# Performance work log

Measured on AMD Instinct MI355X. Metric: run time of the kernel, lower is better.

## Reference

```python
import jax, jax.numpy as jnp
import numpy as np
from math import sqrt

B, S, D, H, E, K, FF = 2, 1024, 1024, 16, 8, 2, 4096
HD = D // H  # 64
EPS = 1e-5


def setup_inputs() -> dict:
    key = jax.random.key(0)
    ks = jax.random.split(key, 20)
    std = 0.02
    p = lambda k, sh: (jax.random.normal(k, sh, dtype=jnp.float32) * std)
    return {
        'x':  jax.random.normal(ks[0], (B, S, D), dtype=jnp.float32),
        'Wq': p(ks[1], (D, D)), 'bq': jnp.zeros((D,), jnp.float32),
        'Wk': p(ks[2], (D, D)), 'bk': jnp.zeros((D,), jnp.float32),
        'Wv': p(ks[3], (D, D)), 'bv': jnp.zeros((D,), jnp.float32),
        'Wo': p(ks[4], (D, D)), 'bo': jnp.zeros((D,), jnp.float32),
        'Wg': p(ks[5], (D, E)), 'bg': jnp.zeros((E,), jnp.float32),
        'W1': p(ks[6], (E, D, FF)), 'b1': jnp.zeros((E, FF), jnp.float32),
        'W2': p(ks[7], (E, FF, D)), 'b2': jnp.zeros((E, D), jnp.float32),
        'g1': jnp.ones((D,), jnp.float32), 'be1': jnp.zeros((D,), jnp.float32),
        'g2': jnp.ones((D,), jnp.float32), 'be2': jnp.zeros((D,), jnp.float32),
    }


def _rope_cache(seq_len, hd):
    inv_freq = 1.0 / (10000.0 ** (jnp.arange(0, hd, 2, dtype=jnp.float32) / hd))
    t = jnp.arange(seq_len, dtype=jnp.float32)
    freqs = t[:, None] * inv_freq[None, :]          # [S, hd/2]
    emb = jnp.concatenate([freqs, freqs], axis=-1)  # [S, hd]
    return jnp.cos(emb), jnp.sin(emb)


def _rotate_half(x):
    x1, x2 = jnp.split(x, 2, axis=-1)
    return jnp.concatenate([-x2, x1], axis=-1)


def _layernorm(x, g, b):
    m = jnp.mean(x, axis=-1, keepdims=True)
    v = jnp.var(x, axis=-1, keepdims=True)
    return (x - m) * jax.lax.rsqrt(v + EPS) * g + b


def _forward(x, Wq, bq, Wk, bk, Wv, bv, Wo, bo, Wg, bg, W1, b1, W2, b2, g1, be1, g2, be2):
    bsz, seq, d = x.shape
    # --- self-attention with RoPE (mask=None -> k=v=q=x) ---
    q = (x @ Wq + bq).reshape(bsz, seq, H, HD).transpose(0, 2, 1, 3)  # [B,H,S,hd]
    k = (x @ Wk + bk).reshape(bsz, seq, H, HD).transpose(0, 2, 1, 3)
    v = (x @ Wv + bv).reshape(bsz, seq, H, HD).transpose(0, 2, 1, 3)
    cos, sin = _rope_cache(seq, HD)                 # [S,hd]
    cos = cos[None, None]; sin = sin[None, None]
    q = q * cos + _rotate_half(q) * sin
    k = k * cos + _rotate_half(k) * sin
    scores = jnp.einsum('bhqd,bhkd->bhqk', q, k) / sqrt(HD)
    attn = jax.nn.softmax(scores, axis=-1)
    ao = jnp.einsum('bhqk,bhkd->bhqd', attn, v)
    ao = ao.transpose(0, 2, 1, 3).reshape(bsz, seq, d)
    attn_out = ao @ Wo + bo
    x1 = _layernorm(x + attn_out, g1, be1)
    # --- MoE: top-k routing, dense-equivalent weighted expert mixture ---
    gate_logits = x1 @ Wg + bg                      # [B,S,E]
    gate_probs = jax.nn.softmax(gate_logits, axis=-1)
    topk_p, topk_i = jax.lax.top_k(gate_probs, K)   # [B,S,K]
    topk_p = topk_p / jnp.sum(topk_p, axis=-1, keepdims=True)
    comb = jnp.sum(jax.nn.one_hot(topk_i, E, dtype=x.dtype) * topk_p[..., None], axis=-2)  # [B,S,E]
    h = jax.nn.gelu(jnp.einsum('bsd,edf->bsef', x1, W1) + b1, approximate=False)  # [B,S,E,FF]
    y = jnp.einsum('bsef,efd->bsed', h, W2) + b2    # [B,S,E,D]
    moe_out = jnp.einsum('bse,bsed->bsd', comb, y)
    return _layernorm(x1 + moe_out, g2, be2)


def reference(x, Wq, bq, Wk, bk, Wv, bv, Wo, bo, Wg, bg, W1, b1, W2, b2, g1, be1, g2, be2):
    return _forward(x, Wq, bq, Wk, bk, Wv, bv, Wo, bo, Wg, bg, W1, b1, W2, b2, g1, be1, g2, be2)
```

## Files before the change

### kernel.cpp

```cpp
#include <hip/hip_runtime.h>
#include <cmath>

#define Bz 2
#define Sz 1024
#define Dz 1024
#define Hz 16
#define HDz 64
#define Ez 8
#define FFz 4096
#define Nz (Bz*Sz)
#define SLOTSz (2*Nz)
#define QKVSz (3*Dz)
#define EPSz 1e-5f
#define NRB 40

typedef __attribute__((ext_vector_type(8))) short bf16x8;
typedef __attribute__((ext_vector_type(4))) short bf16x4;
typedef __attribute__((ext_vector_type(4))) float f32x4;
typedef __attribute__((ext_vector_type(8))) unsigned short ushortx8;

__device__ __forceinline__ float b2f(unsigned short u){
  union { unsigned int i; float f; } x; x.i = ((unsigned int)u) << 16; return x.f;
}
__device__ __forceinline__ unsigned short f2b(float f){
  union { float f; unsigned int i; } x; x.f = f;
  unsigned int r = x.i + 0x7FFFu + ((x.i >> 16) & 1u);
  return (unsigned short)(r >> 16);
}
__device__ __forceinline__ float erf_fast(float x){
  float ax = fabsf(x);
  float t = 1.0f/(1.0f + 0.3275911f*ax);
  float p = t*(0.254829592f + t*(-0.284496736f + t*(1.421413741f +
            t*(-1.453152027f + t*1.061405429f))));
  float r = 1.0f - p*__expf(-ax*ax);
  return copysignf(r, x);
}
__device__ __forceinline__ float gelu_f(float x){
  return 0.5f*x*(1.0f + erf_fast(x*0.70710678118654752f));
}
__device__ __forceinline__ void gload16(const void* g, void* l){
  __builtin_amdgcn_global_load_lds(
    (const __attribute__((address_space(1))) unsigned int*)g,
    (__attribute__((address_space(3))) unsigned int*)l, 16, 0, 0);
}

__device__ __forceinline__ void transpose_body(
    const float* __restrict__ in, unsigned short* __restrict__ out,
    int R, int C, int bx, int by, int tid, float (*tile)[65])
{
  int c0 = bx*64, r0 = by*64;
  int tx = tid & 15, ty = tid >> 4;
  #pragma unroll
  for (int i = 0; i < 4; ++i) {
    float4 v = *(const float4*)(in + (size_t)(r0+ty+16*i)*C + c0 + tx*4);
    tile[ty+16*i][tx*4+0] = v.x; tile[ty+16*i][tx*4+1] = v.y;
    tile[ty+16*i][tx*4+2] = v.z; tile[ty+16*i][tx*4+3] = v.w;
  }
  __syncthreads();
  int oc = tid >> 3, og = tid & 7;
  #pragma unroll
  for (int p = 0; p < 2; ++p) {
    int c = oc + p*32;
    ushortx8 u;
    #pragma unroll
    for (int j = 0; j < 8; ++j) u[j] = f2b(tile[og*8+j][c]);
    *(ushortx8*)(out + (size_t)(c0+c)*R + r0 + og*8) = u;
  }
}

__global__ __launch_bounds__(256) void prologue_k(
    const float* __restrict__ Wq, const float* __restrict__ Wk,
    const float* __restrict__ Wv, const float* __restrict__ Wo,
    const float* __restrict__ bq, const float* __restrict__ bk,
    const float* __restrict__ bv, const float* __restrict__ x,
    unsigned short* __restrict__ Wqt, unsigned short* __restrict__ Wkt,
    unsigned short* __restrict__ Wvt, unsigned short* __restrict__ Wot,
    float* __restrict__ bqkv, unsigned short* __restrict__ xb,
    int* __restrict__ counts)
{
  __shared__ float tile[64][65];
  int id = blockIdx.x, t = threadIdx.x;
  if (id < 1024) {
    int which = id >> 8, rem = id & 255;
    const float* in = (which==0)?Wq:(which==1)?Wk:(which==2)?Wv:Wo;
    unsigned short* out = (which==0)?Wqt:(which==1)?Wkt:(which==2)?Wvt:Wot;
    transpose_body(in, out, Dz, Dz, rem & 15, rem >> 4, t, tile);
  } else if (id < 1024 + 2048) {
    int i = ((id-1024)*256 + t)*4;
    float4 v = *(const float4*)(x + i);
    ushort4 o; o.x=f2b(v.x); o.y=f2b(v.y); o.z=f2b(v.z); o.w=f2b(v.w);
    *(ushort4*)(xb + i) = o;
  } else {
    int i = (id - 3072)*256 + t;
    if (i < 3072) bqkv[i] = (i < 1024) ? bq[i] : (i < 2048 ? bk[i-1024] : bv[i-2048]);
    if (id == 3072 && t < Ez) counts[t] = 0;
  }
}

__device__ __forceinline__ void mfma_kloop(
    const unsigned short* __restrict__ pA0, const unsigned short* __restrict__ pA1,
    const unsigned short* __restrict__ pB0, const unsigned short* __restrict__ pB1,
    char* lds, int t, int K, f32x4 acc[4][4])
{
  const int lane = t & 63, w = t >> 6;
  const int wrOff = (w >> 1) * 4096;
  const int wcOff = (w & 1) * 4096;
  const int lr = lane & 15, q = lane >> 4;
  const int xq = (q ^ (lr & 3)) << 4;
  const int baseA = wrOff + lr*64 + xq;
  const int baseB = 8192 + wcOff + lr*64 + xq;
  for (int k0 = 0; k0 < K; k0 += 32) {
    __syncthreads();
    gload16(pA0 + k0, lds + t*16);
    gload16(pA1 + k0, lds + 4096 + t*16);
    gload16(pB0 + k0, lds + 8192 + t*16);
    gload16(pB1 + k0, lds + 12288 + t*16);
    __syncthreads();
    bf16x8 a[4], b[4];
    #pragma unroll
    for (int m = 0; m < 4; ++m) a[m] = *(const bf16x8*)(lds + baseA + m*1024);
    #pragma unroll
    for (int n = 0; n < 4; ++n) b[n] = *(const bf16x8*)(lds + baseB + n*1024);
    #pragma unroll
    for (int m = 0; m < 4; ++m)
      #pragma unroll
      for (int n = 0; n < 4; ++n)
        acc[m][n] = __builtin_amdgcn_mfma_f32_16x16x32_bf16(a[m], b[n], acc[m][n], 0, 0, 0);
  }
}

__global__ __launch_bounds__(256) void gemm_proj(
    const unsigned short* __restrict__ A, const unsigned short* __restrict__ Bt,
    const float* __restrict__ bias, unsigned short* __restrict__ outb,
    int M, int Nn, int K, int KS, int mode, int doRope)
{
  __shared__ __align__(16) char lds[16384];
  const int t = threadIdx.x;
  const int nblk = Nn >> 7;
  const int chunk = blockIdx.x / nblk;
  const int n0 = (blockIdx.x - chunk*nblk) << 7;
  const int m0 = blockIdx.y << 7;
  const int Kc = K / KS;
  const int kbase = chunk * Kc;
  const int rr = t >> 2;
  const int ch = ((t & 3) ^ (rr & 3)) * 8;
  const unsigned short* pA0 = A + (size_t)(m0 + rr)*K + kbase + ch;
  const unsigned short* pA1 = pA0 + (size_t)64*K;
  const unsigned short* pB0 = Bt + (size_t)(n0 + rr)*K + kbase + ch;
  const unsigned short* pB1 = pB0 + (size_t)64*K;
  f32x4 acc[4][4] = {};
  mfma_kloop(pA0, pA1, pB0, pB1, lds, t, Kc, acc);
  const int lane = t & 63, w = t >> 6;
  const int wr = (w>>1)<<6, wc = (w&1)<<6, lq = lane>>4, lr = lane&15;
  if (mode == 0) {
    #pragma unroll
    for (int m = 0; m < 4; ++m)
      #pragma unroll
      for (int r = 0; r < 4; ++r) {
        int row = m0 + wr + m*16 + lq*4 + r;
        int s = row & (Sz-1);
        #pragma unroll
        for (int n = 0; n < 2; ++n) {
          int col = n0 + wc + n*16 + lr;
          float v0 = acc[m][n][r]   + bias[col];
          float v1 = acc[m][n+2][r] + bias[col+32];
          if (doRope && col < 2*Dz) {
            int i = n*16 + lr;
            float ang = (float)s * __powf(10000.0f, -(float)i*(1.0f/32.0f));
            float sn, cs; __sincosf(ang, &sn, &cs);
            float r0 = v0*cs - v1*sn;
            float r1 = v1*cs + v0*sn;
            v0 = r0; v1 = r1;
          }
          outb[(size_t)row*Nn + col]      = f2b(v0);
          outb[(size_t)row*Nn + col + 32] = f2b(v1);
        }
      }
  } else {
    #pragma unroll
    for (int m = 0; m < 4; ++m)
      #pragma unroll
      for (int r = 0; r < 4; ++r) {
        int row = m0 + wr + m*16 + lq*4 + r;
        #pragma unroll
        for (int n = 0; n < 4; ++n) {
          int col = n0 + wc + n*16 + lr;
          outb[((size_t)chunk*M + row)*Nn + col] = f2b(acc[m][n][r]);
        }
      }
  }
}

__global__ __launch_bounds__(256) void moe_gemm1(
    const unsigned short* __restrict__ x1b, const unsigned short* __restrict__ W1t,
    const float* __restrict__ b1, const int* __restrict__ counts,
    const int* __restrict__ offs, const int* __restrict__ toklist,
    const int2* __restrict__ rbmap, unsigned short* __restrict__ hb)
{
  const int2 rbe = rbmap[blockIdx.y];
  if (rbe.x < 0) return;
  const int e = rbe.x, r0 = rbe.y, cnt = counts[e];
  __shared__ __align__(16) char lds[16384];
  const int t = threadIdx.x, n0 = blockIdx.x*128;
  const int rr = t >> 2;
  const int ch = ((t & 3) ^ (rr & 3)) * 8;
  const int rg0 = r0 + rr, rg1 = r0 + 64 + rr;
  const int tok0 = toklist[e*Nz + (rg0 < cnt ? rg0 : 0)];
  const int tok1 = toklist[e*Nz + (rg1 < cnt ? rg1 : 0)];
  const unsigned short* pA0 = x1b + (size_t)tok0*Dz + ch;
  const unsigned short* pA1 = x1b + (size_t)tok1*Dz + ch;
  const unsigned short* pB0 = W1t + ((size_t)e*FFz + n0 + rr)*Dz + ch;
  const unsigned short* pB1 = pB0 + (size_t)64*Dz;
  f32x4 acc[4][4] = {};
  mfma_kloop(pA0, pA1, pB0, pB1, lds, t, Dz, acc);
  const int lane = t & 63, w = t >> 6;
  const int wr = (w>>1)<<6, wc = (w&1)<<6, lq = lane>>4, lr = lane&15;
  const int base = offs[e] + r0;
  #pragma unroll
  for (int m = 0; m < 4; ++m)
    #pragma unroll
    for (int r = 0; r < 4; ++r) {
      int row = wr + m*16 + lq*4 + r;
      if (r0 + row >= cnt) continue;
      #pragma unroll
      for (int n = 0; n < 4; ++n) {
        int col = n0 + wc + n*16 + lr;
        hb[(size_t)(base+row)*FFz + col] = f2b(gelu_f(acc[m][n][r] + b1[e*FFz + col]));
      }
    }
}

__global__ __launch_bounds__(256) void moe_gemm2(
    const unsigned short* __restrict__ hb, const unsigned short* __restrict__ W2t,
    const int* __restrict__ counts, const int* __restrict__ offs,
    const int2* __restrict__ rbmap, unsigned short* __restrict__ yp)
{
  const int2 rbe = rbmap[blockIdx.y];
  if (rbe.x < 0) return;
  const int e = rbe.x, r0 = rbe.y, cnt = counts[e];
  __shared__ __align__(16) char lds[16384];
  const int t = threadIdx.x;
  const int chunk = blockIdx.x >> 3;
  const int n0 = (blockIdx.x & 7) << 7;
  const int kbase = chunk * (FFz/4);
  const int rr = t >> 2;
  const int ch = ((t & 3) ^ (rr & 3)) * 8;
  const int rg0 = r0 + rr, rg1 = r0 + 64 + rr;
  const int slot0 = offs[e] + (rg0 < cnt ? rg0 : 0);
  const int slot1 = offs[e] + (rg1 < cnt ? rg1 : 0);
  const unsigned short* pA0 = hb + (size_t)slot0*FFz + kbase + ch;
  const unsigned short* pA1 = hb + (size_t)slot1*FFz + kbase + ch;
  const unsigned short* pB0 = W2t + ((size_t)e*Dz + n0 + rr)*FFz + kbase + ch;
  const unsigned short* pB1 = pB0 + (size_t)64*FFz;
  f32x4 acc[4][4] = {};
  mfma_kloop(pA0, pA1, pB0, pB1, lds, t, FFz/4, acc);
  const int lane = t & 63, w = t >> 6;
  const int wr = (w>>1)<<6, wc = (w&1)<<6, lq = lane>>4, lr = lane&15;
  const int base = offs[e] + r0;
  #pragma unroll
  for (int m = 0; m < 4; ++m)
    #pragma unroll
    for (int r = 0; r < 4; ++r) {
      int row = wr + m*16 + lq*4 + r;
      if (r0 + row >= cnt) continue;
      #pragma unroll
      for (int n = 0; n < 4; ++n) {
        int col = n0 + wc + n*16 + lr;
        yp[((size_t)chunk*SLOTSz + base + row)*Dz + col] = f2b(acc[m][n][r]);
      }
    }
}

__global__ __launch_bounds__(256) void mega_k(
    const unsigned short* __restrict__ qkv, unsigned short* __restrict__ ao,
    const float* __restrict__ W1, unsigned short* __restrict__ W1t,
    const float* __restrict__ W2, unsigned short* __restrict__ W2t)
{
  __shared__ __align__(16) char smem[16640];
  const int bid = blockIdx.x;
  if (bid >= 512) {
    if (bid < 512 + 8192) {
      int rem = bid - 512; int e = rem >> 10; int r = rem & 1023;
      transpose_body(W1 + (size_t)e*Dz*FFz, W1t + (size_t)e*FFz*Dz, Dz, FFz,
                     r & 63, r >> 6, threadIdx.x, (float(*)[65])smem);
    } else {
      int rem = bid - 8704; int e = rem >> 10; int r = rem & 1023;
      transpose_body(W2 + (size_t)e*FFz*Dz, W2t + (size_t)e*Dz*FFz, FFz, Dz,
                     r & 15, r >> 4, threadIdx.x, (float(*)[65])smem);
    }
    return;
  }
  const int lb = ((bid & 7) << 6) | (bid >> 3);
  char* Klds = smem;
  char* Vlds = smem + 8192;
  const unsigned short* q = qkv;
  const unsigned short* k = qkv + Dz;
  const unsigned short* v = qkv + 2*Dz;

  const int t = threadIdx.x;
  const int lane = t & 63, w = t >> 6;
  const int p15 = lane & 15, g = lane >> 4;
  const int bh = lb >> 4;
  const int qblk = lb & 15;
  const int b = bh >> 4, h = bh & 15;
  const size_t hoff = (size_t)h*HDz;
  const int q0 = qblk*64 + w*16;

  const size_t qrow = (size_t)(b*Sz + q0 + p15)*QKVSz + hoff;
  const bf16x8 qf0 = *(const bf16x8*)(q + qrow + 8*g);
  const bf16x8 qf1 = *(const bf16x8*)(q + qrow + 32 + 8*g);

  char* Pw = Klds + w*2048;

  float mrun = -INFINITY, lsum = 0.f;
  f32x4 acc_o[4] = {};

  const unsigned short* kbh = k + (size_t)(b*Sz)*QKVSz + hoff;
  const unsigned short* vbh = v + (size_t)(b*Sz)*QKVSz + hoff;

  for (int t0 = 0; t0 < Sz; t0 += 64) {
    __syncthreads();
    #pragma unroll
    for (int u = 0; u < 2; ++u) {
      int j = t + 256*u;
      int kkv = j >> 3, kdc = (j & 7) ^ (kkv & 7);
      gload16(kbh + (size_t)(t0 + kkv)*QKVSz + 8*kdc, Klds + j*16);
      int va = j >> 5, vbb = (j >> 3) & 3, vr = (j >> 1) & 3, vc = 8*(j & 1);
      gload16(vbh + (size_t)(t0 + 4*va + vr)*QKVSz + 16*vbb + vc, Vlds + j*16);
    }
    __syncthreads();

    f32x4 sc[4];
    #pragma unroll
    for (int mt = 0; mt < 4; ++mt) {
      int kv = mt*16 + p15;
      bf16x8 a0 = *(const bf16x8*)(Klds + kv*128 + ((g     ^ (kv & 7))*16));
      bf16x8 a1 = *(const bf16x8*)(Klds + kv*128 + (((g+4) ^ (kv & 7))*16));
      f32x4 z = {};
      z = __builtin_amdgcn_mfma_f32_16x16x32_bf16(a0, qf0, z, 0, 0, 0);
      z = __builtin_amdgcn_mfma_f32_16x16x32_bf16(a1, qf1, z, 0, 0, 0);
      sc[mt] = z;
    }

    float pmax = -INFINITY;
    #pragma unroll
    for (int mt = 0; mt < 4; ++mt)
      #pragma unroll
      for (int r = 0; r < 4; ++r) {
        sc[mt][r] *= 0.125f;
        pmax = fmaxf(pmax, sc[mt][r]);
      }
    pmax = fmaxf(pmax, __shfl_xor(pmax, 16));
    pmax = fmaxf(pmax, __shfl_xor(pmax, 32));
    float mnew = fmaxf(mrun, pmax);
    float resc = __expf(mrun - mnew);
    mrun = mnew;

    __syncthreads();

    float ps = 0.f;
    #pragma unroll
    for (int mt = 0; mt < 4; ++mt) {
      float p0 = __expf(sc[mt][0] - mnew);
      float p1 = __expf(sc[mt][1] - mnew);
      float p2 = __expf(sc[mt][2] - mnew);
      float p3 = __expf(sc[mt][3] - mnew);
      ps += (p0 + p1) + (p2 + p3);
      ushort4 pk;
      pk.x = f2b(p0); pk.y = f2b(p1); pk.z = f2b(p2); pk.w = f2b(p3);
      *(ushort4*)(Pw + ((p15*128 + mt*32 + g*8) ^ ((p15 & 7) << 4))) = pk;
    }
    ps += __shfl_xor(ps, 16);
    ps += __shfl_xor(ps, 32);
    lsum = lsum*resc + ps;
    #pragma unroll
    for (int bb = 0; bb < 4; ++bb) {
      acc_o[bb][0] *= resc; acc_o[bb][1] *= resc;
      acc_o[bb][2] *= resc; acc_o[bb][3] *= resc;
    }

    #pragma unroll
    for (int bb = 0; bb < 4; ++bb) {
      #pragma unroll
      for (int kh = 0; kh < 2; ++kh) {
        const __attribute__((address_space(3))) char* vp =
          (const __attribute__((address_space(3))) char*)
            (Vlds + 4096*kh + 1024*g + 128*bb + 8*p15);
        bf16x4 v0, v1;
        asm volatile("ds_read_b64_tr_b16 %0, %2\n\t"
                     "ds_read_b64_tr_b16 %1, %2 offset:512\n\t"
                     "s_waitcnt lgkmcnt(0)"
                     : "=v"(v0), "=v"(v1) : "v"(vp) : "memory");
        __builtin_amdgcn_sched_barrier(0);
        union { bf16x4 hh[2]; bf16x8 full; } af;
        af.hh[0] = v0; af.hh[1] = v1;
        bf16x8 pf = *(const bf16x8*)(Pw + ((p15*128 + kh*64 + g*16) ^ ((p15 & 7) << 4)));
        acc_o[bb] = __builtin_amdgcn_mfma_f32_16x16x32_bf16(af.full, pf, acc_o[bb], 0, 0, 0);
      }
    }
  }

  const float inv = 1.0f / lsum;
  const size_t orow = (size_t)(b*Sz + q0 + p15)*Dz + hoff;
  #pragma unroll
  for (int bb = 0; bb < 4; ++bb) {
    ushort4 o;
    o.x = f2b(acc_o[bb][0]*inv);
    o.y = f2b(acc_o[bb][1]*inv);
    o.z = f2b(acc_o[bb][2]*inv);
    o.w = f2b(acc_o[bb][3]*inv);
    *(ushort4*)(ao + orow + 16*bb + 4*g) = o;
  }
}

__global__ __launch_bounds__(256) void ln1_k(
    const float* __restrict__ x, const float* __restrict__ bo,
    const unsigned short* __restrict__ op, const float* __restrict__ g,
    const float* __restrict__ beta, const float* __restrict__ Wg,
    const float* __restrict__ bg, float* __restrict__ outf,
    unsigned short* __restrict__ outb, int* __restrict__ counts,
    int* __restrict__ toklist, int4* __restrict__ tokinfo,
    float2* __restrict__ tokw)
{
  int n = blockIdx.x, t = threadIdx.x;
  __shared__ float red[256];
  float vals[4]; float s = 0.f;
  #pragma unroll
  for (int i = 0; i < 4; ++i) {
    int d = t + i*256;
    size_t idx = (size_t)n*Dz + d;
    float p0 = b2f(op[idx]);
    float p1 = b2f(op[(size_t)Nz*Dz + idx]);
    float p2 = b2f(op[(size_t)2*Nz*Dz + idx]);
    float p3 = b2f(op[(size_t)3*Nz*Dz + idx]);
    float xv = x[idx] + bo[d] + ((p0 + p1) + (p2 + p3));
    vals[i] = xv; s += xv;
  }
  red[t] = s; __syncthreads();
  for (int st = 128; st; st >>= 1) { if (t < st) red[t] += red[t+st]; __syncthreads(); }
  float mean = red[0] * (1.0f/Dz);
  __syncthreads();
  float vsum = 0.f;
  #pragma unroll
  for (int i = 0; i < 4; ++i){ float dd = vals[i]-mean; vsum += dd*dd; }
  red[t] = vsum; __syncthreads();
  for (int st = 128; st; st >>= 1) { if (t < st) red[t] += red[t+st]; __syncthreads(); }
  float rs = rsqrtf(red[0]*(1.0f/Dz) + EPSz);
  float ga[8] = {0,0,0,0,0,0,0,0};
  #pragma unroll
  for (int i = 0; i < 4; ++i) {
    int d = t + i*256;
    float o = (vals[i]-mean)*rs*g[d] + beta[d];
    outf[(size_t)n*Dz + d] = o;
    outb[(size_t)n*Dz + d] = f2b(o);
    const float4* wp = (const float4*)(Wg + (size_t)d*Ez);
    float4 w0 = wp[0], w1 = wp[1];
    ga[0] += o*w0.x; ga[1] += o*w0.y; ga[2] += o*w0.z; ga[3] += o*w0.w;
    ga[4] += o*w1.x; ga[5] += o*w1.y; ga[6] += o*w1.z; ga[7] += o*w1.w;
  }
  #pragma unroll
  for (int e = 0; e < 8; ++e)
    #pragma unroll
    for (int off = 32; off; off >>= 1) ga[e] += __shfl_xor(ga[e], off);
  __syncthreads();
  if ((t & 63) == 0) {
    #pragma unroll
    for (int e = 0; e < 8; ++e) red[(t >> 6)*8 + e] = ga[e];
  }
  __syncthreads();
  if (t == 0) {
    float lg[8]; float mx = -INFINITY;
    #pragma unroll
    for (int e = 0; e < 8; ++e){
      lg[e] = (red[e] + red[8+e]) + (red[16+e] + red[24+e]) + bg[e];
      mx = fmaxf(mx, lg[e]);
    }
    float p[8];
    #pragma unroll
    for (int e = 0; e < 8; ++e) p[e] = __expf(lg[e]-mx);
    int e1 = 0; float m1 = p[0];
    for (int e = 1; e < 8; ++e) if (p[e] > m1){ m1 = p[e]; e1 = e; }
    int e2 = -1; float m2 = -INFINITY;
    for (int e = 0; e < 8; ++e) if (e != e1 && p[e] > m2){ m2 = p[e]; e2 = e; }
    float inv = 1.0f/(m1+m2);
    int p1 = atomicAdd(&counts[e1], 1); toklist[e1*Nz + p1] = n;
    int p2 = atomicAdd(&counts[e2], 1); toklist[e2*Nz + p2] = n;
    tokinfo[n] = make_int4(e1, p1, e2, p2);
    tokw[n] = make_float2(m1*inv, m2*inv);
  }
}

__global__ void prefix_k(const int* __restrict__ counts, int* __restrict__ offs,
                         int2* __restrict__ rbmap){
  if (threadIdx.x == 0 && blockIdx.x == 0) {
    int s = 0;
    for (int e = 0; e < Ez; ++e){ offs[e] = s; s += counts[e]; }
    offs[Ez] = s;
    int rb = 0;
    for (int e = 0; e < Ez; ++e) {
      int nrb = (counts[e] + 127) >> 7;
      for (int i = 0; i < nrb; ++i) rbmap[rb++] = make_int2(e, i*128);
    }
    for (; rb < NRB; ++rb) rbmap[rb] = make_int2(-1, 0);
  }
}

__global__ __launch_bounds__(256) void ln2_k(
    const float* __restrict__ x1, const unsigned short* __restrict__ yp,
    const float* __restrict__ b2, const int4* __restrict__ tokinfo,
    const float2* __restrict__ tokw, const int* __restrict__ offs,
    const float* __restrict__ g, const float* __restrict__ beta,
    float* __restrict__ out)
{
  int n = blockIdx.x, t = threadIdx.x;
  __shared__ float red[256];
  int4 ti = tokinfo[n]; float2 tw = tokw[n];
  const size_t s1 = (size_t)(offs[ti.x] + ti.y)*Dz;
  const size_t s2 = (size_t)(offs[ti.z] + ti.w)*Dz;
  const size_t CS = (size_t)SLOTSz*Dz;
  const float* b2a = b2 + (size_t)ti.x*Dz;
  const float* b2b = b2 + (size_t)ti.z*Dz;
  float vals[4]; float s = 0.f;
  #pragma unroll
  for (int i = 0; i < 4; ++i) {
    int d = t + i*256;
    float a0 = b2f(yp[s1 + d]);
    float a1 = b2f(yp[CS + s1 + d]);
    float a2 = b2f(yp[2*CS + s1 + d]);
    float a3 = b2f(yp[3*CS + s1 + d]);
    float c0 = b2f(yp[s2 + d]);
    float c1 = b2f(yp[CS + s2 + d]);
    float c2 = b2f(yp[2*CS + s2 + d]);
    float c3 = b2f(yp[3*CS + s2 + d]);
    float sumA = (a0 + a1) + (a2 + a3);
    float sumB = (c0 + c1) + (c2 + c3);
    float xv = x1[(size_t)n*Dz + d] + tw.x*(sumA + b2a[d]) + tw.y*(sumB + b2b[d]);
    vals[i] = xv; s += xv;
  }
  red[t] = s; __syncthreads();
  for (int st = 128; st; st >>= 1) { if (t < st) red[t] += red[t+st]; __syncthreads(); }
  float mean = red[0] * (1.0f/Dz);
  __syncthreads();
  float vsum = 0.f;
  #pragma unroll
  for (int i = 0; i < 4; ++i){ float dd = vals[i]-mean; vsum += dd*dd; }
  red[t] = vsum; __syncthreads();
  for (int st = 128; st; st >>= 1) { if (t < st) red[t] += red[t+st]; __syncthreads(); }
  float rs = rsqrtf(red[0]*(1.0f/Dz) + EPSz);
  #pragma unroll
  for (int i = 0; i < 4; ++i) {
    int d = t + i*256;
    out[(size_t)n*Dz + d] = (vals[i]-mean)*rs*g[d] + beta[d];
  }
}

extern "C" void kernel_launch(void* const* d_in, const int* in_sizes, int n_in,
                              void* d_out, int out_size, void* d_ws, size_t ws_size,
                              hipStream_t stream)
{
  const float* x  = (const float*)d_in[0];
  const float* Wq = (const float*)d_in[1];
  const float* bq = (const float*)d_in[2];
  const float* Wk = (const float*)d_in[3];
  const float* bk = (const float*)d_in[4];
  const float* Wv = (const float*)d_in[5];
  const float* bv = (const float*)d_in[6];
  const float* Wo = (const float*)d_in[7];
  const float* bo = (const float*)d_in[8];
  const float* Wg = (const float*)d_in[9];
  const float* bg = (const float*)d_in[10];
  const float* W1 = (const float*)d_in[11];
  const float* b1 = (const float*)d_in[12];
  const float* W2 = (const float*)d_in[13];
  const float* b2 = (const float*)d_in[14];
  const float* g1 = (const float*)d_in[15];
  const float* be1= (const float*)d_in[16];
  const float* g2 = (const float*)d_in[17];
  const float* be2= (const float*)d_in[18];
  float* out = (float*)d_out;

  const size_t PD = (size_t)Dz*Dz;
  const size_t ND = (size_t)Nz*Dz;
  unsigned short* Wqt = (unsigned short*)d_ws;
  unsigned short* Wkt = Wqt + PD;
  unsigned short* Wvt = Wkt + PD;
  unsigned short* Wot = Wvt + PD;
  unsigned short* W1t = Wot + PD;
  unsigned short* W2t = W1t + (size_t)Ez*FFz*Dz;
  unsigned short* hb  = W2t + (size_t)Ez*FFz*Dz;
  unsigned short* xb  = hb  + (size_t)SLOTSz*FFz;
  unsigned short* qkvb= xb  + ND;
  unsigned short* aob = qkvb + (size_t)Nz*QKVSz;
  unsigned short* x1b = aob + ND;
  float* x1 = (float*)(x1b + ND);
  unsigned short* yp = (unsigned short*)(x1 + ND);
  unsigned short* op = yp;
  float* bqkv = (float*)(yp + (size_t)4*SLOTSz*Dz);
  int4*  tokinfo = (int4*)(bqkv + QKVSz);
  float2* tokw   = (float2*)(tokinfo + Nz);
  int* counts  = (int*)(tokw + Nz);
  int* offs    = counts + Ez;
  int* toklist = offs + Ez + 1;
  int2* rbmap  = (int2*)(toklist + Ez*Nz);

  dim3 blk(256);
  prologue_k<<<3084, blk, 0, stream>>>(Wq, Wk, Wv, Wo, bq, bk, bv, x,
                                       Wqt, Wkt, Wvt, Wot, bqkv, xb, counts);

  gemm_proj<<<dim3(QKVSz/128, Nz/128), blk, 0, stream>>>(
      xb, Wqt, bqkv, qkvb, Nz, QKVSz, Dz, 1, 0, 1);

  mega_k<<<512 + 2*8192, blk, 0, stream>>>(qkvb, aob, W1, W1t, W2, W2t);

  gemm_proj<<<dim3((Dz/128)*4, Nz/128), blk, 0, stream>>>(
      aob, Wot, nullptr, op, Nz, Dz, Dz, 4, 1, 0);

  ln1_k<<<Nz, blk, 0, stream>>>(x, bo, op, g1, be1, Wg, bg, x1, x1b,
                                counts, toklist, tokinfo, tokw);
  prefix_k<<<1, dim3(64), 0, stream>>>(counts, offs, rbmap);
  moe_gemm1<<<dim3(FFz/128, NRB), blk, 0, stream>>>(x1b, W1t, b1, counts, offs, toklist, rbmap, hb);
  moe_gemm2<<<dim3((Dz/128)*4, NRB), blk, 0, stream>>>(hb, W2t, counts, offs, rbmap, yp);
  ln2_k<<<Nz, blk, 0, stream>>>(x1, yp, b2, tokinfo, tokw, offs, g2, be2, out);
}
```

Baseline: 354.1 us.

## Triple-buffer LDS in shared MFMA k-loop with async prefetch two tiles ahead

The shared GEMM k-loop now uses three 16KB LDS buffers and issues direct-to-LDS global loads two k-steps ahead. Raw s_waitcnt vmcnt(4) plus s_barrier replaces the two __syncthreads per iteration, so global loads overlap MFMA compute. LDS per block grows from 16KB to 48KB, which may cut the number of resident blocks per CU. The correctness of the vmcnt counting depends on gload16 issuing exactly one vm op per call.

```diff
diff --git a/kernel.cpp b/kernel.cpp
--- a/kernel.cpp
+++ b/kernel.cpp
@@ -109,24 +109,47 @@
   const int xq = (q ^ (lr & 3)) << 4;
   const int baseA = wrOff + lr*64 + xq;
   const int baseB = 8192 + wcOff + lr*64 + xq;
-  for (int k0 = 0; k0 < K; k0 += 32) {
-    __syncthreads();
-    gload16(pA0 + k0, lds + t*16);
-    gload16(pA1 + k0, lds + 4096 + t*16);
-    gload16(pB0 + k0, lds + 8192 + t*16);
-    gload16(pB1 + k0, lds + 12288 + t*16);
-    __syncthreads();
+#define STAGEK(bi, k0) do { \
+    char* _b = lds + (bi)*16384; \
+    gload16(pA0 + (k0), _b + t*16); \
+    gload16(pA1 + (k0), _b + 4096 + t*16); \
+    gload16(pB0 + (k0), _b + 8192 + t*16); \
+    gload16(pB1 + (k0), _b + 12288 + t*16); \
+  } while(0)
+#define WAITBAR4 do { __builtin_amdgcn_sched_barrier(0); \
+    asm volatile("s_waitcnt vmcnt(4) lgkmcnt(0)\n\ts_barrier" ::: "memory"); \
+    __builtin_amdgcn_sched_barrier(0); } while(0)
+#define WAITBAR0 do { __builtin_amdgcn_sched_barrier(0); \
+    asm volatile("s_waitcnt vmcnt(0) lgkmcnt(0)\n\ts_barrier" ::: "memory"); \
+    __builtin_amdgcn_sched_barrier(0); } while(0)
+  const int nt = K >> 5;
+  STAGEK(0, 0);
+  if (nt > 1) { STAGEK(1, 32); WAITBAR4; }
+  else        {                WAITBAR0; }
+  int cur = 0;
+  for (int ti = 0; ti < nt; ++ti) {
+    const bool more = (ti + 2 < nt);
+    if (more) {
+      int stg = cur + 2; if (stg >= 3) stg -= 3;
+      STAGEK(stg, (ti + 2) << 5);
+    }
+    char* cb = lds + cur*16384;
     bf16x8 a[4], b[4];
     #pragma unroll
-    for (int m = 0; m < 4; ++m) a[m] = *(const bf16x8*)(lds + baseA + m*1024);
-    #pragma unroll
-    for (int n = 0; n < 4; ++n) b[n] = *(const bf16x8*)(lds + baseB + n*1024);
+    for (int m = 0; m < 4; ++m) a[m] = *(const bf16x8*)(cb + baseA + m*1024);
+    #pragma unroll
+    for (int n = 0; n < 4; ++n) b[n] = *(const bf16x8*)(cb + baseB + n*1024);
     #pragma unroll
     for (int m = 0; m < 4; ++m)
       #pragma unroll
       for (int n = 0; n < 4; ++n)
         acc[m][n] = __builtin_amdgcn_mfma_f32_16x16x32_bf16(a[m], b[n], acc[m][n], 0, 0, 0);
-  }
+    if (more) WAITBAR4; else WAITBAR0;
+    cur += 1; if (cur >= 3) cur -= 3;
+  }
+#undef STAGEK
+#undef WAITBAR4
+#undef WAITBAR0
 }
 
 __global__ __launch_bounds__(256) void gemm_proj(
@@ -134,7 +157,7 @@
     const float* __restrict__ bias, unsigned short* __restrict__ outb,
     int M, int Nn, int K, int KS, int mode, int doRope)
 {
-  __shared__ __align__(16) char lds[16384];
+  __shared__ __align__(16) char lds[49152];
   const int t = threadIdx.x;
   const int nblk = Nn >> 7;
   const int chunk = blockIdx.x / nblk;
@@ -200,7 +223,7 @@
   const int2 rbe = rbmap[blockIdx.y];
   if (rbe.x < 0) return;
   const int e = rbe.x, r0 = rbe.y, cnt = counts[e];
-  __shared__ __align__(16) char lds[16384];
+  __shared__ __align__(16) char lds[49152];
   const int t = threadIdx.x, n0 = blockIdx.x*128;
   const int rr = t >> 2;
   const int ch = ((t & 3) ^ (rr & 3)) * 8;
@@ -238,7 +261,7 @@
   const int2 rbe = rbmap[blockIdx.y];
   if (rbe.x < 0) return;
   const int e = rbe.x, r0 = rbe.y, cnt = counts[e];
-  __shared__ __align__(16) char lds[16384];
+  __shared__ __align__(16) char lds[49152];
   const int t = threadIdx.x;
   const int chunk = blockIdx.x >> 3;
   const int n0 = (blockIdx.x & 7) << 7;
```

Result: faster. 333.8 us (-5.7%).
